# Kernel optimization log

Hardware: AMD Instinct MI355X
Metric: run time of the kernel (lower is better)

## Reference

```python
import jax, jax.numpy as jnp
import numpy as np
import math

D = 256; H = 8; L = 4; P = 4; DH = D // H; DF = 1024
B = 16; Q = 512
T_SHAPES = [8192, 4096, 2048, 1024]
LSI = [0, 8192, 12288, 14336]
S = sum(T_SHAPES)
EPS = 1e-5


def ln(x, w, b):
    m = jnp.mean(x, -1, keepdims=True)
    v = jnp.mean((x - m) ** 2, -1, keepdims=True)
    return (x - m) / jnp.sqrt(v + EPS) * w + b


def mha(q, k, v, valid, in_w, in_b, out_w, out_b):
    b_, n, _ = q.shape
    wq, wk, wv = jnp.split(in_w, 3, axis=0)
    bq, bk, bv = jnp.split(in_b, 3)
    qh = (q @ wq.T + bq).reshape(b_, n, H, DH).transpose(0, 2, 1, 3)
    kh = (k @ wk.T + bk).reshape(b_, n, H, DH).transpose(0, 2, 1, 3)
    vh = (v @ wv.T + bv).reshape(b_, n, H, DH).transpose(0, 2, 1, 3)
    s = jnp.einsum('bhqd,bhkd->bhqk', qh, kh) / math.sqrt(DH)
    s = jnp.where(valid[:, None, None, :], s, -1e30)
    a = jax.nn.softmax(s, -1)
    o = jnp.einsum('bhqk,bhkd->bhqd', a, vh).transpose(0, 2, 1, 3).reshape(b_, n, D)
    return o @ out_w.T + out_b


def msda(query, ref, src, pad_mask, ow, ob, aw, ab, vw, vb, pw, pb):
    # 1D multiscale deformable attention (PDVC-style), grid_sample semantics
    # with align_corners=False and zero padding.
    b_, s_, _ = src.shape
    q_ = query.shape[1]
    val = jnp.where(pad_mask[..., None], 0.0, src @ vw.T + vb).reshape(b_, s_, H, DH)
    off = (query @ ow.T + ob).reshape(b_, q_, H, L, P)
    attn = jax.nn.softmax((query @ aw.T + ab).reshape(b_, q_, H, L * P), -1)
    attn = attn.reshape(b_, q_, H, L, P)
    shapes = jnp.asarray(T_SHAPES, query.dtype)
    # (b,q,H,L,P) normalized sampling locations in [0,1]
    loc = ref[:, :, None, :, None, 0] + off / shapes[None, None, None, :, None]
    out = jnp.zeros((b_, q_, H, DH), query.dtype)
    for l in range(L):
        T = T_SHAPES[l]
        v = val[:, LSI[l]:LSI[l] + T].transpose(0, 2, 1, 3)  # (b,H,T,DH)
        x = loc[:, :, :, l, :] * T - 0.5  # pixel coords (b,q,H,P)
        x0 = jnp.floor(x)
        w = x - x0
        i0 = x0.astype(jnp.int32)
        i1 = i0 + 1
        m0 = ((i0 >= 0) & (i0 < T)).astype(query.dtype)
        m1 = ((i1 >= 0) & (i1 < T)).astype(query.dtype)

        def gather(idx):
            idxr = jnp.clip(idx, 0, T - 1).transpose(0, 2, 1, 3).reshape(b_, H, q_ * P)
            g = jnp.take_along_axis(v, idxr[..., None], axis=2)  # (b,H,q*P,DH)
            return g.reshape(b_, H, q_, P, DH).transpose(0, 2, 1, 3, 4)

        samp = gather(i0) * (m0 * (1.0 - w))[..., None] + gather(i1) * (m1 * w)[..., None]
        out = out + jnp.einsum('bqhp,bqhpd->bqhd', attn[:, :, :, l, :], samp)
    return out.reshape(b_, q_, D) @ pw.T + pb, loc[..., None], attn


def layer_fwd(tgt, query_pos, ref_v, ref_a, query_mask, vsrc, vpad, asrc, apad, p):
    qk = tgt + query_pos
    t2 = mha(qk, qk, tgt, query_mask, p['sa_in_w'], p['sa_in_b'], p['sa_out_w'], p['sa_out_b'])
    t = ln(tgt + t2, p['n2_w'], p['n2_b'])
    qv = t + query_pos
    ca_args = (p['ca_off_w'], p['ca_off_b'], p['ca_attn_w'], p['ca_attn_b'],
               p['ca_val_w'], p['ca_val_b'], p['ca_out_w'], p['ca_out_b'])
    cv, vloc, vattn = msda(qv, ref_v, vsrc, vpad, *ca_args)
    tv = ln(t + cv, p['n1_w'], p['n1_b'])
    ca, aloc, aattn = msda(qv, ref_a, asrc, apad, *ca_args)
    ta = ln(t + ca, p['n1_w'], p['n1_b'])
    cat = ln(jnp.concatenate([tv, ta], -1), p['n4_w'], p['n4_b'])
    x = jax.nn.relu(cat @ p['lin3_w'].T + p['lin3_b'])
    ff = jax.nn.relu(x @ p['lin1_w'].T + p['lin1_b']) @ p['lin2_w'].T + p['lin2_b']
    out = ln(x + ff, p['n3_w'], p['n3_b'])
    return out, tv, ta, vloc, vattn, aloc, aattn


def setup_inputs() -> dict:
    key = jax.random.key(0)
    ks = jax.random.split(key, 24)
    g = lambda k, shp: (jax.random.normal(k, shp, jnp.float32) * 0.02)
    inp = {
        'tgt': jax.random.normal(ks[0], (B, Q, D), jnp.float32),
        'query_pos': jax.random.normal(ks[1], (B, Q, D), jnp.float32),
        'reference_points_input_video': jax.random.uniform(ks[2], (B, Q, L, 1), jnp.float32),
        'reference_points_input_audio': jax.random.uniform(ks[3], (B, Q, L, 1), jnp.float32),
        'query_mask': jnp.ones((B, Q), bool),
        'video_src': jax.random.normal(ks[4], (B, S, D), jnp.float32),
        'video_temporal_shapes': jnp.asarray(T_SHAPES, jnp.int64),
        'video_level_start_index': jnp.asarray(LSI, jnp.int64),
        'video_src_padding_mask': jnp.zeros((B, S), bool),
        'audio_src': jax.random.normal(ks[5], (B, S, D), jnp.float32),
        'audio_temporal_shapes': jnp.asarray(T_SHAPES, jnp.int64),
        'audio_level_start_index': jnp.asarray(LSI, jnp.int64),
        'audio_src_padding_mask': jnp.zeros((B, S), bool),
        'sa_in_w': g(ks[6], (3 * D, D)), 'sa_in_b': jnp.zeros((3 * D,), jnp.float32),
        'sa_out_w': g(ks[7], (D, D)), 'sa_out_b': jnp.zeros((D,), jnp.float32),
        'ca_off_w': g(ks[8], (H * L * P, D)), 'ca_off_b': jax.random.uniform(ks[9], (H * L * P,), jnp.float32, -4.0, 4.0),
        'ca_attn_w': g(ks[10], (H * L * P, D)), 'ca_attn_b': jnp.zeros((H * L * P,), jnp.float32),
        'ca_val_w': g(ks[11], (D, D)), 'ca_val_b': jnp.zeros((D,), jnp.float32),
        'ca_out_w': g(ks[12], (D, D)), 'ca_out_b': jnp.zeros((D,), jnp.float32),
        'n1_w': jnp.ones((D,), jnp.float32), 'n1_b': jnp.zeros((D,), jnp.float32),
        'n2_w': jnp.ones((D,), jnp.float32), 'n2_b': jnp.zeros((D,), jnp.float32),
        'n3_w': jnp.ones((D,), jnp.float32), 'n3_b': jnp.zeros((D,), jnp.float32),
        'n4_w': jnp.ones((2 * D,), jnp.float32), 'n4_b': jnp.zeros((2 * D,), jnp.float32),
        'lin1_w': g(ks[13], (DF, D)), 'lin1_b': jnp.zeros((DF,), jnp.float32),
        'lin2_w': g(ks[14], (D, DF)), 'lin2_b': jnp.zeros((D,), jnp.float32),
        'lin3_w': g(ks[15], (D, 2 * D)), 'lin3_b': jnp.zeros((D,), jnp.float32),
    }
    return inp


def reference(tgt, query_pos, reference_points_input_video, reference_points_input_audio,
              query_mask, video_src, video_temporal_shapes, video_level_start_index,
              video_src_padding_mask, audio_src, audio_temporal_shapes,
              audio_level_start_index, audio_src_padding_mask,
              sa_in_w, sa_in_b, sa_out_w, sa_out_b,
              ca_off_w, ca_off_b, ca_attn_w, ca_attn_b, ca_val_w, ca_val_b, ca_out_w, ca_out_b,
              n1_w, n1_b, n2_w, n2_b, n3_w, n3_b, n4_w, n4_b,
              lin1_w, lin1_b, lin2_w, lin2_b, lin3_w, lin3_b):
    p = dict(sa_in_w=sa_in_w, sa_in_b=sa_in_b, sa_out_w=sa_out_w, sa_out_b=sa_out_b,
             ca_off_w=ca_off_w, ca_off_b=ca_off_b, ca_attn_w=ca_attn_w, ca_attn_b=ca_attn_b,
             ca_val_w=ca_val_w, ca_val_b=ca_val_b, ca_out_w=ca_out_w, ca_out_b=ca_out_b,
             n1_w=n1_w, n1_b=n1_b, n2_w=n2_w, n2_b=n2_b, n3_w=n3_w, n3_b=n3_b,
             n4_w=n4_w, n4_b=n4_b, lin1_w=lin1_w, lin1_b=lin1_b,
             lin2_w=lin2_w, lin2_b=lin2_b, lin3_w=lin3_w, lin3_b=lin3_b)
    return layer_fwd(tgt, query_pos, reference_points_input_video,
                     reference_points_input_audio, query_mask,
                     video_src, video_src_padding_mask,
                     audio_src, audio_src_padding_mask, p)
```

## Files before the change

### kernel.cpp

```cpp
#include <hip/hip_runtime.h>
#include <hip/hip_bf16.h>
#include <cstddef>

#define Dm   256
#define Hh   8
#define Bb   16
#define Qq   512
#define Ss   15360
#define TOK  (Bb*Qq)
#define VROWS (Bb*Ss)
#define EPSf 1e-5f
#define SCALEf 0.17677669529663687f

typedef __attribute__((ext_vector_type(8))) short bf16x8;
typedef __attribute__((ext_vector_type(4))) float f32x4;

__device__ __forceinline__ unsigned short rne_bf16(float f) {
    unsigned int u = __builtin_bit_cast(unsigned int, f);
    u += 0x7fffu + ((u >> 16) & 1u);
    return (unsigned short)(u >> 16);
}
__device__ __forceinline__ float bf2f(unsigned short u) {
    return __builtin_bit_cast(float, (unsigned int)u << 16);
}

struct WcArgs { const float* src[9]; };

__global__ __launch_bounds__(256) void wconv_kernel(
    WcArgs a, unsigned short* __restrict__ dst,
    const float* __restrict__ offb, const float* __restrict__ attnb,
    float* __restrict__ bias_oa)
{
    if (blockIdx.x == 1088) {
        int t = threadIdx.x;
        bias_oa[t] = (t < 128) ? offb[t] : attnb[t - 128];
        return;
    }
    int g = blockIdx.x * 256 + threadIdx.x;
    const int pre[10] = {0, 49152, 65536, 73728, 81920, 98304, 114688, 147456, 212992, 278528};
    int seg = 0;
    #pragma unroll
    for (int s2 = 1; s2 < 9; ++s2) seg += (g >= pre[s2]);
    float4 f = reinterpret_cast<const float4*>(a.src[seg])[g - pre[seg]];
    ushort4 o;
    o.x = rne_bf16(f.x); o.y = rne_bf16(f.y);
    o.z = rne_bf16(f.z); o.w = rne_bf16(f.w);
    reinterpret_cast<ushort4*>(dst)[g] = o;
}

template<int BM, int BN, bool RELU, bool ABF, bool OBF, bool ADD, bool SPLITA>
__global__ __launch_bounds__(512) void gemm_mfma_kernel(
    const void* __restrict__ Ap, const void* __restrict__ Ap2,
    const float* __restrict__ A2,
    const unsigned short* __restrict__ W,
    const float* __restrict__ bias, void* __restrict__ Cp,
    int M, int N, int K, int Msplit)
{
    constexpr int MI = BM / 32;
    constexpr int NI = BN / 64;
    __shared__ unsigned short As[BM * 32];
    __shared__ unsigned short Bs[BN * 32];
    const int tid = threadIdx.x, wid = tid >> 6, lane = tid & 63;
    const int wr = wid >> 2, wc = wid & 3;
    const int bm = blockIdx.x * BM, bn = blockIdx.y * BN;
    const int l15 = lane & 15, l4 = lane >> 4;
    const void* Ause = Ap;
    int bmA = bm;
    if (SPLITA && bm >= Msplit) { Ause = Ap2; bmA = bm - Msplit; }
    f32x4 acc[MI][NI] = {};

    for (int k0 = 0; k0 < K; k0 += 32) {
        __syncthreads();
        if (ABF) {
            const unsigned short* A = (const unsigned short*)Ause;
            constexpr int CH = BM * 4;
            #pragma unroll
            for (int i = 0; i < (CH + 511) / 512; ++i) {
                int idx = i * 512 + tid;
                if ((CH % 512) && idx >= CH) break;
                int row = idx >> 2, c = idx & 3;
                int4 a4 = *reinterpret_cast<const int4*>(&A[(size_t)(bmA + row) * K + k0 + c * 8]);
                *reinterpret_cast<int4*>(reinterpret_cast<char*>(As)
                    + row * 64 + ((c ^ (row & 3)) << 4)) = a4;
            }
        } else {
            const float* A = (const float*)Ause;
            constexpr int CH = BM * 8;
            #pragma unroll
            for (int i = 0; i < CH / 512; ++i) {
                int idx = i * 512 + tid;
                int row = idx >> 3, c4 = idx & 7;
                size_t g = (size_t)(bmA + row) * K + k0 + c4 * 4;
                float4 a4 = *reinterpret_cast<const float4*>(&A[g]);
                if (ADD) {
                    float4 b4 = *reinterpret_cast<const float4*>(
                        &A2[(size_t)(bm + row) * K + k0 + c4 * 4]);
                    a4.x += b4.x; a4.y += b4.y; a4.z += b4.z; a4.w += b4.w;
                }
                ushort4 u;
                u.x = rne_bf16(a4.x); u.y = rne_bf16(a4.y);
                u.z = rne_bf16(a4.z); u.w = rne_bf16(a4.w);
                *reinterpret_cast<ushort4*>(reinterpret_cast<char*>(As)
                    + row * 64 + (((c4 >> 1) ^ (row & 3)) << 4) + (c4 & 1) * 8) = u;
            }
        }
        {
            constexpr int CH = BN * 4;
            #pragma unroll
            for (int i = 0; i < CH / 512; ++i) {
                int idx = i * 512 + tid;
                int row = idx >> 2, c = idx & 3;
                int4 w4 = *reinterpret_cast<const int4*>(&W[(size_t)(bn + row) * K + k0 + c * 8]);
                *reinterpret_cast<int4*>(reinterpret_cast<char*>(Bs)
                    + row * 64 + ((c ^ (row & 3)) << 4)) = w4;
            }
        }
        __syncthreads();
        bf16x8 af[MI], bfr[NI];
        #pragma unroll
        for (int i = 0; i < MI; ++i) {
            int r = wr * (BM / 2) + i * 16 + l15;
            af[i] = *reinterpret_cast<const bf16x8*>(
                reinterpret_cast<const char*>(As) + r * 64 + ((l4 ^ (r & 3)) << 4));
        }
        #pragma unroll
        for (int j = 0; j < NI; ++j) {
            int r = wc * (BN / 4) + j * 16 + l15;
            bfr[j] = *reinterpret_cast<const bf16x8*>(
                reinterpret_cast<const char*>(Bs) + r * 64 + ((l4 ^ (r & 3)) << 4));
        }
        #pragma unroll
        for (int i = 0; i < MI; ++i)
            #pragma unroll
            for (int j = 0; j < NI; ++j)
                acc[i][j] = __builtin_amdgcn_mfma_f32_16x16x32_bf16(
                    af[i], bfr[j], acc[i][j], 0, 0, 0);
    }
    #pragma unroll
    for (int j = 0; j < NI; ++j) {
        int col = bn + wc * (BN / 4) + j * 16 + l15;
        float bv = bias[col];
        #pragma unroll
        for (int i = 0; i < MI; ++i) {
            int row0 = bm + wr * (BM / 2) + i * 16 + l4 * 4;
            #pragma unroll
            for (int v = 0; v < 4; ++v) {
                float val = acc[i][j][v] + bv;
                if (RELU) val = fmaxf(val, 0.f);
                if (OBF)
                    ((unsigned short*)Cp)[(size_t)(row0 + v) * N + col] = rne_bf16(val);
                else
                    ((float*)Cp)[(size_t)(row0 + v) * N + col] = val;
            }
        }
    }
}

template<int BM, bool DUAL>
__global__ __launch_bounds__(512) void gemm_ln_kernel(
    const unsigned short* __restrict__ A,
    const unsigned short* __restrict__ W,
    const float* __restrict__ bias,
    const float* __restrict__ res,
    const float* __restrict__ lnw, const float* __restrict__ lnb,
    float* __restrict__ out0, float* __restrict__ out1,
    int M, int K)
{
    constexpr int MI = BM / 32;
    constexpr int NI = 4;
    __shared__ unsigned short As[BM * 32];
    __shared__ unsigned short Bs[256 * 32];
    __shared__ float redS[BM][4];
    __shared__ float redQ[BM][4];
    const int tid = threadIdx.x, wid = tid >> 6, lane = tid & 63;
    const int wr = wid >> 2, wc = wid & 3;
    const int bm = blockIdx.x * BM;
    const int l15 = lane & 15, l4 = lane >> 4;
    f32x4 acc[MI][NI] = {};

    for (int k0 = 0; k0 < K; k0 += 32) {
        __syncthreads();
        {
            constexpr int CH = BM * 4;
            #pragma unroll
            for (int i = 0; i < (CH + 511) / 512; ++i) {
                int idx = i * 512 + tid;
                if ((CH % 512) && idx >= CH) break;
                int row = idx >> 2, c = idx & 3;
                int4 a4 = *reinterpret_cast<const int4*>(&A[(size_t)(bm + row) * K + k0 + c * 8]);
                *reinterpret_cast<int4*>(reinterpret_cast<char*>(As)
                    + row * 64 + ((c ^ (row & 3)) << 4)) = a4;
            }
        }
        {
            #pragma unroll
            for (int i = 0; i < 2; ++i) {
                int idx = i * 512 + tid;
                int row = idx >> 2, c = idx & 3;
                int4 w4 = *reinterpret_cast<const int4*>(&W[(size_t)row * K + k0 + c * 8]);
                *reinterpret_cast<int4*>(reinterpret_cast<char*>(Bs)
                    + row * 64 + ((c ^ (row & 3)) << 4)) = w4;
            }
        }
        __syncthreads();
        bf16x8 af[MI], bfr[NI];
        #pragma unroll
        for (int i = 0; i < MI; ++i) {
            int r = wr * (BM / 2) + i * 16 + l15;
            af[i] = *reinterpret_cast<const bf16x8*>(
                reinterpret_cast<const char*>(As) + r * 64 + ((l4 ^ (r & 3)) << 4));
        }
        #pragma unroll
        for (int j = 0; j < NI; ++j) {
            int r = wc * 64 + j * 16 + l15;
            bfr[j] = *reinterpret_cast<const bf16x8*>(
                reinterpret_cast<const char*>(Bs) + r * 64 + ((l4 ^ (r & 3)) << 4));
        }
        #pragma unroll
        for (int i = 0; i < MI; ++i)
            #pragma unroll
            for (int j = 0; j < NI; ++j)
                acc[i][j] = __builtin_amdgcn_mfma_f32_16x16x32_bf16(
                    af[i], bfr[j], acc[i][j], 0, 0, 0);
    }

    const bool hi = DUAL && (bm >= (M >> 1));
    const int bmL = hi ? bm - (M >> 1) : bm;
    float* outp = (DUAL && hi) ? out1 : out0;

    #pragma unroll
    for (int i = 0; i < MI; ++i) {
        #pragma unroll
        for (int v = 0; v < 4; ++v) {
            int rloc = wr * (BM / 2) + i * 16 + l4 * 4 + v;
            size_t rrow = (size_t)(bmL + rloc) * 256;
            float s = 0.f, q = 0.f;
            #pragma unroll
            for (int j = 0; j < NI; ++j) {
                int col = wc * 64 + j * 16 + l15;
                float x = acc[i][j][v] + bias[col] + res[rrow + col];
                acc[i][j][v] = x;
                s += x; q += x * x;
            }
            #pragma unroll
            for (int msk = 1; msk < 16; msk <<= 1) {
                s += __shfl_xor(s, msk, 64);
                q += __shfl_xor(q, msk, 64);
            }
            if (l15 == 0) { redS[rloc][wc] = s; redQ[rloc][wc] = q; }
        }
    }
    __syncthreads();
    #pragma unroll
    for (int i = 0; i < MI; ++i) {
        #pragma unroll
        for (int v = 0; v < 4; ++v) {
            int rloc = wr * (BM / 2) + i * 16 + l4 * 4 + v;
            float S = redS[rloc][0] + redS[rloc][1] + redS[rloc][2] + redS[rloc][3];
            float Qs = redQ[rloc][0] + redQ[rloc][1] + redQ[rloc][2] + redQ[rloc][3];
            float mean = S * (1.f / 256.f);
            float var = Qs * (1.f / 256.f) - mean * mean;
            float rinv = rsqrtf(var + EPSf);
            size_t rrow = (size_t)(bmL + rloc) * 256;
            #pragma unroll
            for (int j = 0; j < NI; ++j) {
                int col = wc * 64 + j * 16 + l15;
                outp[rrow + col] = (acc[i][j][v] - mean) * rinv * lnw[col] + lnb[col];
            }
        }
    }
}

__global__ __launch_bounds__(512) void gemm_prep_kernel(
    const float* __restrict__ A, const float* __restrict__ A2,
    const unsigned short* __restrict__ W, const float* __restrict__ bias,
    const float* __restrict__ refv, const float* __restrict__ refa,
    float* __restrict__ vloc, float* __restrict__ vattn,
    float* __restrict__ aloc, float* __restrict__ aattn)
{
    constexpr int BM = 64, MI = 2, NI = 4;
    const int K = 256;
    __shared__ unsigned short As[BM * 32];
    __shared__ unsigned short Bs[256 * 32];
    const int tid = threadIdx.x, wid = tid >> 6, lane = tid & 63;
    const int wr = wid >> 2, wc = wid & 3;
    const int bm = blockIdx.x * BM;
    const int l15 = lane & 15, l4 = lane >> 4;
    f32x4 acc[MI][NI] = {};

    for (int k0 = 0; k0 < K; k0 += 32) {
        __syncthreads();
        {
            int idx = tid;
            int row = idx >> 3, c4 = idx & 7;
            size_t g = (size_t)(bm + row) * K + k0 + c4 * 4;
            float4 a4 = *reinterpret_cast<const float4*>(&A[g]);
            float4 b4 = *reinterpret_cast<const float4*>(&A2[g]);
            a4.x += b4.x; a4.y += b4.y; a4.z += b4.z; a4.w += b4.w;
            ushort4 u;
            u.x = rne_bf16(a4.x); u.y = rne_bf16(a4.y);
            u.z = rne_bf16(a4.z); u.w = rne_bf16(a4.w);
            *reinterpret_cast<ushort4*>(reinterpret_cast<char*>(As)
                + row * 64 + (((c4 >> 1) ^ (row & 3)) << 4) + (c4 & 1) * 8) = u;
        }
        {
            #pragma unroll
            for (int i = 0; i < 2; ++i) {
                int idx = i * 512 + tid;
                int row = idx >> 2, c = idx & 3;
                int4 w4 = *reinterpret_cast<const int4*>(&W[(size_t)row * K + k0 + c * 8]);
                *reinterpret_cast<int4*>(reinterpret_cast<char*>(Bs)
                    + row * 64 + ((c ^ (row & 3)) << 4)) = w4;
            }
        }
        __syncthreads();
        bf16x8 af[MI], bfr[NI];
        #pragma unroll
        for (int i = 0; i < MI; ++i) {
            int r = wr * 32 + i * 16 + l15;
            af[i] = *reinterpret_cast<const bf16x8*>(
                reinterpret_cast<const char*>(As) + r * 64 + ((l4 ^ (r & 3)) << 4));
        }
        #pragma unroll
        for (int j = 0; j < NI; ++j) {
            int r = wc * 64 + j * 16 + l15;
            bfr[j] = *reinterpret_cast<const bf16x8*>(
                reinterpret_cast<const char*>(Bs) + r * 64 + ((l4 ^ (r & 3)) << 4));
        }
        #pragma unroll
        for (int i = 0; i < MI; ++i)
            #pragma unroll
            for (int j = 0; j < NI; ++j)
                acc[i][j] = __builtin_amdgcn_mfma_f32_16x16x32_bf16(
                    af[i], bfr[j], acc[i][j], 0, 0, 0);
    }

    const float invT[4] = {1.f/8192.f, 1.f/4096.f, 1.f/2048.f, 1.f/1024.f};
    const int l = (l15 >> 2) & 3;
    if (wc < 2) {
        #pragma unroll
        for (int i = 0; i < MI; ++i) {
            #pragma unroll
            for (int v = 0; v < 4; ++v) {
                int tok = bm + wr * 32 + i * 16 + l4 * 4 + v;
                float rv = refv[(size_t)tok * 4 + l];
                float ra = refa[(size_t)tok * 4 + l];
                #pragma unroll
                for (int j = 0; j < NI; ++j) {
                    int col = wc * 64 + j * 16 + l15;
                    float off = (acc[i][j][v] + bias[col]) * invT[l];
                    vloc[(size_t)tok * 128 + col] = rv + off;
                    aloc[(size_t)tok * 128 + col] = ra + off;
                }
            }
        }
    } else {
        #pragma unroll
        for (int i = 0; i < MI; ++i) {
            #pragma unroll
            for (int v = 0; v < 4; ++v) {
                int tok = bm + wr * 32 + i * 16 + l4 * 4 + v;
                #pragma unroll
                for (int j = 0; j < NI; ++j) {
                    int col = wc * 64 + j * 16 + l15;
                    float lg = acc[i][j][v] + bias[col];
                    float m = lg;
                    #pragma unroll
                    for (int msk = 1; msk < 16; msk <<= 1)
                        m = fmaxf(m, __shfl_xor(m, msk, 64));
                    float e = __expf(lg - m);
                    float s = e;
                    #pragma unroll
                    for (int msk = 1; msk < 16; msk <<= 1)
                        s += __shfl_xor(s, msk, 64);
                    float at = e / s;
                    int c = col - 128;
                    vattn[(size_t)tok * 128 + c] = at;
                    aattn[(size_t)tok * 128 + c] = at;
                }
            }
        }
    }
}

__global__ __launch_bounds__(256) void sa_flash_kernel(
    const unsigned short* __restrict__ qkh, const unsigned short* __restrict__ vh,
    unsigned short* __restrict__ o)
{
    const int qt = blockIdx.x & 3;
    const int h  = (blockIdx.x >> 2) & 7;
    const int b  = blockIdx.x >> 5;
    const int tid = threadIdx.x;
    const int wid = tid >> 6;
    const int lane = tid & 63;
    const int l15 = lane & 15, l4 = lane >> 4;

    __shared__ unsigned short Ks[64 * 32];
    __shared__ unsigned short Vt[32 * 64];
    __shared__ unsigned short Ps[4][32 * 64];

    const int qbase = qt * 128 + wid * 32;
    bf16x8 qf[2];
    #pragma unroll
    for (int i = 0; i < 2; ++i) {
        int row = b * 512 + qbase + i * 16 + l15;
        qf[i] = *reinterpret_cast<const bf16x8*>(&qkh[(size_t)row * 512 + h * 32 + l4 * 8]);
    }

    f32x4 oacc[2][2] = {};
    float m_r[8], l_r[8];
    #pragma unroll
    for (int i = 0; i < 8; ++i) { m_r[i] = -1e30f; l_r[i] = 0.f; }

    for (int kt = 0; kt < 8; ++kt) {
        __syncthreads();
        {
            int row = tid >> 2, c = tid & 3;
            int4 k4 = *reinterpret_cast<const int4*>(
                &qkh[(size_t)(b * 512 + kt * 64 + row) * 512 + 256 + h * 32 + c * 8]);
            *reinterpret_cast<int4*>(reinterpret_cast<char*>(Ks)
                + row * 64 + ((c ^ (row & 3)) << 4)) = k4;
        }
        {
            int k = tid >> 2, dh0 = (tid & 3) * 8;
            const unsigned short* vp = &vh[(size_t)(b * 512 + kt * 64 + k) * 256 + h * 32 + dh0];
            ushort4 v0 = *reinterpret_cast<const ushort4*>(vp);
            ushort4 v1 = *reinterpret_cast<const ushort4*>(vp + 4);
            unsigned short vv[8] = {v0.x, v0.y, v0.z, v0.w, v1.x, v1.y, v1.z, v1.w};
            int kc = k >> 3, kb = (k & 7) * 2;
            #pragma unroll
            for (int j = 0; j < 8; ++j) {
                int dh = dh0 + j;
                *reinterpret_cast<unsigned short*>(reinterpret_cast<char*>(Vt)
                    + dh * 128 + ((kc ^ (dh & 7)) << 4) + kb) = vv[j];
            }
        }
        __syncthreads();

        bf16x8 kf[4];
        #pragma unroll
        for (int j = 0; j < 4; ++j) {
            int r = j * 16 + l15;
            kf[j] = *reinterpret_cast<const bf16x8*>(
                reinterpret_cast<const char*>(Ks) + r * 64 + ((l4 ^ (r & 3)) << 4));
        }
        f32x4 s[2][4];
        #pragma unroll
        for (int i = 0; i < 2; ++i)
            #pragma unroll
            for (int j = 0; j < 4; ++j) {
                f32x4 z = {0.f, 0.f, 0.f, 0.f};
                s[i][j] = __builtin_amdgcn_mfma_f32_16x16x32_bf16(qf[i], kf[j], z, 0, 0, 0);
            }

        #pragma unroll
        for (int i = 0; i < 2; ++i) {
            #pragma unroll
            for (int reg = 0; reg < 4; ++reg) {
                float v0 = s[i][0][reg] * SCALEf;
                float v1 = s[i][1][reg] * SCALEf;
                float v2 = s[i][2][reg] * SCALEf;
                float v3 = s[i][3][reg] * SCALEf;
                float mx = fmaxf(fmaxf(v0, v1), fmaxf(v2, v3));
                #pragma unroll
                for (int d = 1; d < 16; d <<= 1) mx = fmaxf(mx, __shfl_xor(mx, d, 64));
                int idx = i * 4 + reg;
                float mnew = fmaxf(m_r[idx], mx);
                float alpha = __expf(m_r[idx] - mnew);
                float p0 = __expf(v0 - mnew), p1 = __expf(v1 - mnew);
                float p2 = __expf(v2 - mnew), p3 = __expf(v3 - mnew);
                float rs = (p0 + p1) + (p2 + p3);
                #pragma unroll
                for (int d = 1; d < 16; d <<= 1) rs += __shfl_xor(rs, d, 64);
                l_r[idx] = l_r[idx] * alpha + rs;
                m_r[idx] = mnew;
                oacc[i][0][reg] *= alpha;
                oacc[i][1][reg] *= alpha;
                int row = i * 16 + l4 * 4 + reg;
                char* pbase = reinterpret_cast<char*>(Ps[wid]) + row * 128 + (l15 & 7) * 2;
                int ch = l15 >> 3;
                unsigned short pb[4] = {rne_bf16(p0), rne_bf16(p1), rne_bf16(p2), rne_bf16(p3)};
                #pragma unroll
                for (int j = 0; j < 4; ++j)
                    *reinterpret_cast<unsigned short*>(
                        pbase + (((j * 2 + ch) ^ (row & 7)) << 4)) = pb[j];
            }
        }
        asm volatile("s_waitcnt lgkmcnt(0)" ::: "memory");
        __builtin_amdgcn_sched_barrier(0);

        #pragma unroll
        for (int ks = 0; ks < 2; ++ks) {
            bf16x8 vf[2], pf[2];
            #pragma unroll
            for (int jd = 0; jd < 2; ++jd) {
                int r = jd * 16 + l15;
                vf[jd] = *reinterpret_cast<const bf16x8*>(
                    reinterpret_cast<const char*>(Vt) + r * 128 + (((ks * 4 + l4) ^ (r & 7)) << 4));
            }
            #pragma unroll
            for (int i = 0; i < 2; ++i) {
                int r = i * 16 + l15;
                pf[i] = *reinterpret_cast<const bf16x8*>(
                    reinterpret_cast<const char*>(Ps[wid]) + r * 128 + (((ks * 4 + l4) ^ (r & 7)) << 4));
            }
            #pragma unroll
            for (int i = 0; i < 2; ++i)
                #pragma unroll
                for (int jd = 0; jd < 2; ++jd)
                    oacc[i][jd] = __builtin_amdgcn_mfma_f32_16x16x32_bf16(
                        pf[i], vf[jd], oacc[i][jd], 0, 0, 0);
        }
    }

    #pragma unroll
    for (int i = 0; i < 2; ++i)
        #pragma unroll
        for (int reg = 0; reg < 4; ++reg) {
            int idx = i * 4 + reg;
            float inv = 1.f / l_r[idx];
            int qrow = b * 512 + qbase + i * 16 + l4 * 4 + reg;
            #pragma unroll
            for (int jd = 0; jd < 2; ++jd)
                o[(size_t)qrow * 256 + h * 32 + jd * 16 + l15] =
                    rne_bf16(oacc[i][jd][reg] * inv);
        }
}

__global__ __launch_bounds__(256) void cat_ln_kernel(
    const float* __restrict__ tv, const float* __restrict__ ta,
    const float* __restrict__ w, const float* __restrict__ beta,
    unsigned short* __restrict__ out)
{
    const int tok = blockIdx.x;
    const int t = threadIdx.x;
    const float x0 = tv[(size_t)tok * 256 + t];
    const float x1 = ta[(size_t)tok * 256 + t];
    __shared__ float red[8];
    float s = x0 + x1;
    #pragma unroll
    for (int k = 32; k > 0; k >>= 1) s += __shfl_xor(s, k, 64);
    if ((t & 63) == 0) red[t >> 6] = s;
    __syncthreads();
    const float mean = (red[0] + red[1] + red[2] + red[3]) * (1.f / 512.f);
    const float d0 = x0 - mean, d1 = x1 - mean;
    float v = d0 * d0 + d1 * d1;
    #pragma unroll
    for (int k = 32; k > 0; k >>= 1) v += __shfl_xor(v, k, 64);
    if ((t & 63) == 0) red[4 + (t >> 6)] = v;
    __syncthreads();
    const float var = (red[4] + red[5] + red[6] + red[7]) * (1.f / 512.f);
    const float r = 1.f / sqrtf(var + EPSf);
    out[(size_t)tok * 512 + t]       = rne_bf16(d0 * r * w[t] + beta[t]);
    out[(size_t)tok * 512 + 256 + t] = rne_bf16(d1 * r * w[256 + t] + beta[256 + t]);
}

__global__ __launch_bounds__(256) void msda_sample_kernel(
    const unsigned short* __restrict__ val,
    const float* __restrict__ vloc, const float* __restrict__ vattn,
    const float* __restrict__ aloc, const float* __restrict__ aattn,
    unsigned short* __restrict__ out)
{
    const int t = threadIdx.x;
    const int tq = t >> 6;
    const int h  = (t >> 3) & 7;
    const int d4 = t & 7;
    const int tok2 = blockIdx.x * 4 + tq;
    const int mod = tok2 >> 13;
    const int tok = tok2 & 8191;
    const int b = tok >> 9;
    const float* loc  = mod ? aloc  : vloc;
    const float* attn = mod ? aattn : vattn;
    const unsigned short* vbase = val + (size_t)mod * VROWS * 256
                                + (size_t)b * Ss * 256 + h * 32 + d4 * 4;
    const int Tt[4]   = {8192, 4096, 2048, 1024};
    const int LSIc[4] = {0, 8192, 12288, 14336};
    float4 acc = {0.f, 0.f, 0.f, 0.f};
    #pragma unroll
    for (int l = 0; l < 4; ++l) {
        const unsigned short* vl = vbase + (size_t)LSIc[l] * 256;
        const int T = Tt[l];
        #pragma unroll
        for (int p = 0; p < 4; ++p) {
            const int e = (h * 4 + l) * 4 + p;
            const float lc = loc[(size_t)tok * 128 + e];
            const float at = attn[(size_t)tok * 128 + e];
            const float x = lc * (float)T - 0.5f;
            const float x0 = floorf(x);
            const float w = x - x0;
            const int i0 = (int)x0;
            const int i1 = i0 + 1;
            const float w0 = (i0 >= 0 && i0 < T) ? at * (1.f - w) : 0.f;
            const float w1 = (i1 >= 0 && i1 < T) ? at * w : 0.f;
            const int i0c = min(max(i0, 0), T - 1);
            const int i1c = min(max(i1, 0), T - 1);
            ushort4 g0 = *reinterpret_cast<const ushort4*>(&vl[(size_t)i0c * 256]);
            ushort4 g1 = *reinterpret_cast<const ushort4*>(&vl[(size_t)i1c * 256]);
            acc.x += w0 * bf2f(g0.x) + w1 * bf2f(g1.x);
            acc.y += w0 * bf2f(g0.y) + w1 * bf2f(g1.y);
            acc.z += w0 * bf2f(g0.z) + w1 * bf2f(g1.z);
            acc.w += w0 * bf2f(g0.w) + w1 * bf2f(g1.w);
        }
    }
    ushort4 ov;
    ov.x = rne_bf16(acc.x); ov.y = rne_bf16(acc.y);
    ov.z = rne_bf16(acc.z); ov.w = rne_bf16(acc.w);
    *reinterpret_cast<ushort4*>(&out[(size_t)tok2 * 256 + h * 32 + d4 * 4]) = ov;
}

extern "C" void kernel_launch(void* const* d_in, const int* in_sizes, int n_in,
                              void* d_out, int out_size, void* d_ws, size_t ws_size,
                              hipStream_t stream)
{
    (void)in_sizes; (void)n_in; (void)out_size; (void)ws_size;
    const float* tgt       = (const float*)d_in[0];
    const float* query_pos = (const float*)d_in[1];
    const float* ref_v     = (const float*)d_in[2];
    const float* ref_a     = (const float*)d_in[3];
    const float* video_src = (const float*)d_in[5];
    const float* audio_src = (const float*)d_in[9];
    const float* sa_in_w   = (const float*)d_in[13];
    const float* sa_in_b   = (const float*)d_in[14];
    const float* sa_out_w  = (const float*)d_in[15];
    const float* sa_out_b  = (const float*)d_in[16];
    const float* ca_off_w  = (const float*)d_in[17];
    const float* ca_off_b  = (const float*)d_in[18];
    const float* ca_attn_w = (const float*)d_in[19];
    const float* ca_attn_b = (const float*)d_in[20];
    const float* ca_val_w  = (const float*)d_in[21];
    const float* ca_val_b  = (const float*)d_in[22];
    const float* ca_out_w  = (const float*)d_in[23];
    const float* ca_out_b  = (const float*)d_in[24];
    const float* n1_w = (const float*)d_in[25];
    const float* n1_b = (const float*)d_in[26];
    const float* n2_w = (const float*)d_in[27];
    const float* n2_b = (const float*)d_in[28];
    const float* n3_w = (const float*)d_in[29];
    const float* n3_b = (const float*)d_in[30];
    const float* n4_w = (const float*)d_in[31];
    const float* n4_b = (const float*)d_in[32];
    const float* lin1_w = (const float*)d_in[33];
    const float* lin1_b = (const float*)d_in[34];
    const float* lin2_w = (const float*)d_in[35];
    const float* lin2_b = (const float*)d_in[36];
    const float* lin3_w = (const float*)d_in[37];
    const float* lin3_b = (const float*)d_in[38];

    float* out_main  = (float*)d_out;
    float* out_tv    = out_main + (size_t)TOK * 256;
    float* out_ta    = out_tv   + (size_t)TOK * 256;
    float* out_vloc  = out_ta   + (size_t)TOK * 256;
    float* out_vattn = out_vloc + (size_t)TOK * 128;
    float* out_aloc  = out_vattn+ (size_t)TOK * 128;
    float* out_aattn = out_aloc + (size_t)TOK * 128;

    char* base = (char*)d_ws;
    const size_t MB = 1024 * 1024;
    unsigned short* f_qkh = (unsigned short*)(base + 0);
    unsigned short* f_vh  = (unsigned short*)(base + 8*MB);
    unsigned short* f_o   = (unsigned short*)(base + 12*MB);
    unsigned short* f_samp= (unsigned short*)(base + 0);
    unsigned short* f_cat = (unsigned short*)(base + 8*MB);
    unsigned short* f_ffh = (unsigned short*)(base + 16*MB);
    float* f_t = (float*)(base + 32*MB);
    float* f_x = (float*)(base + 40*MB);
    unsigned short* f_val = (unsigned short*)(base + 48*MB);
    unsigned short* wb = (unsigned short*)(base + 300*MB);
    unsigned short* w_sa_in  = wb;
    unsigned short* w_sa_out = w_sa_in  + 768 * 256;
    unsigned short* w_oa     = w_sa_out + 256 * 256;
    unsigned short* w_val    = w_oa     + 256 * 256;
    unsigned short* w_caout  = w_val    + 256 * 256;
    unsigned short* w_lin3   = w_caout  + 256 * 256;
    unsigned short* w_lin1   = w_lin3   + 256 * 512;
    unsigned short* w_lin2   = w_lin1   + 1024 * 256;
    float* bias_oa = (float*)(w_lin2 + 256 * 1024);

    WcArgs wa;
    wa.src[0] = sa_in_w;  wa.src[1] = sa_out_w; wa.src[2] = ca_off_w;
    wa.src[3] = ca_attn_w;wa.src[4] = ca_val_w; wa.src[5] = ca_out_w;
    wa.src[6] = lin3_w;   wa.src[7] = lin1_w;   wa.src[8] = lin2_w;
    hipLaunchKernelGGL(wconv_kernel, dim3(1089), dim3(256), 0, stream,
                       wa, wb, ca_off_b, ca_attn_b, bias_oa);

    hipLaunchKernelGGL((gemm_mfma_kernel<64,128,false,false,true,true,false>),
                       dim3(128, 4), dim3(512), 0, stream,
                       tgt, nullptr, query_pos, w_sa_in, sa_in_b, f_qkh,
                       TOK, 512, 256, 0);
    hipLaunchKernelGGL((gemm_mfma_kernel<64,128,false,false,true,false,false>),
                       dim3(128, 2), dim3(512), 0, stream,
                       tgt, nullptr, nullptr, w_sa_in + (size_t)512 * 256,
                       sa_in_b + 512, f_vh, TOK, 256, 256, 0);
    hipLaunchKernelGGL(sa_flash_kernel, dim3(Bb * 32), dim3(256), 0, stream,
                       f_qkh, f_vh, f_o);
    hipLaunchKernelGGL((gemm_ln_kernel<32,false>), dim3(256), dim3(512), 0, stream,
                       f_o, w_sa_out, sa_out_b, tgt, n2_w, n2_b,
                       f_t, nullptr, TOK, 256);
    hipLaunchKernelGGL(gemm_prep_kernel, dim3(128), dim3(512), 0, stream,
                       f_t, query_pos, w_oa, bias_oa, ref_v, ref_a,
                       out_vloc, out_vattn, out_aloc, out_aattn);
    hipLaunchKernelGGL((gemm_mfma_kernel<128,256,false,false,true,false,true>),
                       dim3(2 * VROWS / 128, 1), dim3(512), 0, stream,
                       video_src, audio_src, nullptr, w_val, ca_val_b, f_val,
                       2 * VROWS, 256, 256, VROWS);
    hipLaunchKernelGGL(msda_sample_kernel, dim3(2 * TOK / 4), dim3(256), 0, stream,
                       f_val, out_vloc, out_vattn, out_aloc, out_aattn, f_samp);
    hipLaunchKernelGGL((gemm_ln_kernel<64,true>), dim3(256), dim3(512), 0, stream,
                       f_samp, w_caout, ca_out_b, f_t, n1_w, n1_b,
                       out_tv, out_ta, 2 * TOK, 256);
    hipLaunchKernelGGL(cat_ln_kernel, dim3(TOK), dim3(256), 0, stream,
                       out_tv, out_ta, n4_w, n4_b, f_cat);
    hipLaunchKernelGGL((gemm_mfma_kernel<64,128,true,true,false,false,false>),
                       dim3(128, 2), dim3(512), 0, stream,
                       f_cat, nullptr, nullptr, w_lin3, lin3_b, f_x,
                       TOK, 256, 512, 0);
    hipLaunchKernelGGL((gemm_mfma_kernel<128,256,true,false,true,false,false>),
                       dim3(64, 4), dim3(512), 0, stream,
                       f_x, nullptr, nullptr, w_lin1, lin1_b, f_ffh,
                       TOK, 1024, 256, 0);
    hipLaunchKernelGGL((gemm_ln_kernel<32,false>), dim3(256), dim3(512), 0, stream,
                       f_ffh, w_lin2, lin2_b, f_x, n3_w, n3_b,
                       out_main, nullptr, TOK, 1024);
}
```

Before: 437.0 us.

## Add streaming value-projection kernel with whole weight resident in LDS

```diff
diff --git a/kernel.cpp b/kernel.cpp
--- a/kernel.cpp
+++ b/kernel.cpp
@@ -46,6 +46,69 @@
     o.x = rne_bf16(f.x); o.y = rne_bf16(f.y);
     o.z = rne_bf16(f.z); o.w = rne_bf16(f.w);
     reinterpret_cast<ushort4*>(dst)[g] = o;
+}
+
+__global__ __launch_bounds__(1024, 4) void val_stream_kernel(
+    const float* __restrict__ Av, const float* __restrict__ Aa,
+    const unsigned short* __restrict__ W, const float* __restrict__ bias,
+    unsigned short* __restrict__ C)
+{
+    __shared__ unsigned short Ws[8 * 256 * 32];
+    const int tid = threadIdx.x;
+    #pragma unroll
+    for (int i = 0; i < 8; ++i) {
+        int g = i * 1024 + tid;
+        int r = g >> 5, q = g & 31;
+        int c = q >> 2, ck = q & 3;
+        int slot = ck ^ (r & 3) ^ ((r >> 2) & 3);
+        int4 w4 = reinterpret_cast<const int4*>(W)[g];
+        *reinterpret_cast<int4*>(reinterpret_cast<char*>(Ws)
+            + c * 16384 + r * 64 + (slot << 4)) = w4;
+    }
+    __syncthreads();
+
+    const int wid = tid >> 6, lane = tid & 63;
+    const int l15 = lane & 15, l4 = lane >> 4;
+    size_t grow = (size_t)blockIdx.x * 256 + wid * 16;
+    const float* A = Av;
+    size_t arow = grow;
+    if (grow >= (size_t)VROWS) { A = Aa; arow = grow - VROWS; }
+    const float* aptr = A + (arow + l15) * 256 + l4 * 8;
+
+    f32x4 acc[16] = {};
+    float4 a0 = *reinterpret_cast<const float4*>(aptr);
+    float4 a1 = *reinterpret_cast<const float4*>(aptr + 4);
+    #pragma unroll
+    for (int kc = 0; kc < 8; ++kc) {
+        float4 n0, n1;
+        if (kc < 7) {
+            n0 = *reinterpret_cast<const float4*>(aptr + (kc + 1) * 32);
+            n1 = *reinterpret_cast<const float4*>(aptr + (kc + 1) * 32 + 4);
+        }
+        bf16x8 af;
+        af[0] = (short)rne_bf16(a0.x); af[1] = (short)rne_bf16(a0.y);
+        af[2] = (short)rne_bf16(a0.z); af[3] = (short)rne_bf16(a0.w);
+        af[4] = (short)rne_bf16(a1.x); af[5] = (short)rne_bf16(a1.y);
+        af[6] = (short)rne_bf16(a1.z); af[7] = (short)rne_bf16(a1.w);
+        const char* wbase = reinterpret_cast<const char*>(Ws) + kc * 16384;
+        #pragma unroll
+        for (int n = 0; n < 16; ++n) {
+            int r = n * 16 + l15;
+            int slot = l4 ^ (r & 3) ^ ((r >> 2) & 3);
+            bf16x8 bf = *reinterpret_cast<const bf16x8*>(wbase + r * 64 + (slot << 4));
+            acc[n] = __builtin_amdgcn_mfma_f32_16x16x32_bf16(af, bf, acc[n], 0, 0, 0);
+        }
+        if (kc < 7) { a0 = n0; a1 = n1; }
+    }
+    #pragma unroll
+    for (int n = 0; n < 16; ++n) {
+        int col = n * 16 + l15;
+        float bv = bias[col];
+        size_t r0 = grow + l4 * 4;
+        #pragma unroll
+        for (int v = 0; v < 4; ++v)
+            C[(r0 + v) * 256 + col] = rne_bf16(acc[n][v] + bv);
+    }
 }
 
 template<int BM, int BN, bool RELU, bool ABF, bool OBF, bool ADD, bool SPLITA>
@@ -699,10 +762,8 @@
     hipLaunchKernelGGL(gemm_prep_kernel, dim3(128), dim3(512), 0, stream,
                        f_t, query_pos, w_oa, bias_oa, ref_v, ref_a,
                        out_vloc, out_vattn, out_aloc, out_aattn);
-    hipLaunchKernelGGL((gemm_mfma_kernel<128,256,false,false,true,false,true>),
-                       dim3(2 * VROWS / 128, 1), dim3(512), 0, stream,
-                       video_src, audio_src, nullptr, w_val, ca_val_b, f_val,
-                       2 * VROWS, 256, 256, VROWS);
+    hipLaunchKernelGGL(val_stream_kernel, dim3(2 * VROWS / 256), dim3(1024), 0, stream,
+                       video_src, audio_src, w_val, ca_val_b, f_val);
     hipLaunchKernelGGL(msda_sample_kernel, dim3(2 * TOK / 4), dim3(256), 0, stream,
                        f_val, out_vloc, out_vattn, out_aloc, out_aattn, f_samp);
     hipLaunchKernelGGL((gemm_ln_kernel<64,true>), dim3(256), dim3(512), 0, stream,
```

After: 399.2 us. 8.7% less time.

## Replace value-projection GEMM with persistent streaming kernel holding weights in registers

Applied to the files above, without the earlier changes.

```diff
diff --git a/kernel.cpp b/kernel.cpp
--- a/kernel.cpp
+++ b/kernel.cpp
@@ -46,6 +46,98 @@
     o.x = rne_bf16(f.x); o.y = rne_bf16(f.y);
     o.z = rne_bf16(f.z); o.w = rne_bf16(f.w);
     reinterpret_cast<ushort4*>(dst)[g] = o;
+}
+
+__global__ __launch_bounds__(512, 2) void val_stream_kernel(
+    const float* __restrict__ Av, const float* __restrict__ Aa,
+    const unsigned short* __restrict__ W, const float* __restrict__ bias,
+    unsigned short* __restrict__ C)
+{
+    const int tid = threadIdx.x, wid = tid >> 6, lane = tid & 63;
+    const int l15 = lane & 15, l4 = lane >> 4;
+    const int rg = wid >> 2;
+    const int cg = wid & 3;
+
+    bf16x8 wf[4][8];
+    #pragma unroll
+    for (int j = 0; j < 4; ++j)
+        #pragma unroll
+        for (int kc = 0; kc < 8; ++kc)
+            wf[j][kc] = *reinterpret_cast<const bf16x8*>(
+                &W[(size_t)(cg * 64 + j * 16 + l15) * 256 + kc * 32 + l4 * 8]);
+    float4 bb[4];
+    #pragma unroll
+    for (int j = 0; j < 4; ++j)
+        bb[j] = *reinterpret_cast<const float4*>(&bias[cg * 64 + j * 16 + l4 * 4]);
+
+    int t = blockIdx.x;
+    const float* ap;
+    {
+        size_t grow = (size_t)t * 32;
+        const float* A = (grow < (size_t)VROWS) ? Av : Aa;
+        size_t ar = (grow < (size_t)VROWS) ? grow : grow - VROWS;
+        ap = A + (ar + rg * 16 + l15) * 256 + l4 * 8;
+    }
+
+    float4 b0[4], b1[4];
+    #define LOADQ(buf, base, ph) {                                          \
+        buf[0] = *reinterpret_cast<const float4*>((base) + (ph) * 64);      \
+        buf[1] = *reinterpret_cast<const float4*>((base) + (ph) * 64 + 4);  \
+        buf[2] = *reinterpret_cast<const float4*>((base) + (ph) * 64 + 32); \
+        buf[3] = *reinterpret_cast<const float4*>((base) + (ph) * 64 + 36); }
+    #define COMPQ(buf, kc0) {                                               \
+        bf16x8 a0, a1;                                                      \
+        a0[0] = (short)rne_bf16(buf[0].x); a0[1] = (short)rne_bf16(buf[0].y); \
+        a0[2] = (short)rne_bf16(buf[0].z); a0[3] = (short)rne_bf16(buf[0].w); \
+        a0[4] = (short)rne_bf16(buf[1].x); a0[5] = (short)rne_bf16(buf[1].y); \
+        a0[6] = (short)rne_bf16(buf[1].z); a0[7] = (short)rne_bf16(buf[1].w); \
+        acc[0] = __builtin_amdgcn_mfma_f32_16x16x32_bf16(wf[0][kc0], a0, acc[0], 0, 0, 0); \
+        acc[1] = __builtin_amdgcn_mfma_f32_16x16x32_bf16(wf[1][kc0], a0, acc[1], 0, 0, 0); \
+        acc[2] = __builtin_amdgcn_mfma_f32_16x16x32_bf16(wf[2][kc0], a0, acc[2], 0, 0, 0); \
+        acc[3] = __builtin_amdgcn_mfma_f32_16x16x32_bf16(wf[3][kc0], a0, acc[3], 0, 0, 0); \
+        a1[0] = (short)rne_bf16(buf[2].x); a1[1] = (short)rne_bf16(buf[2].y); \
+        a1[2] = (short)rne_bf16(buf[2].z); a1[3] = (short)rne_bf16(buf[2].w); \
+        a1[4] = (short)rne_bf16(buf[3].x); a1[5] = (short)rne_bf16(buf[3].y); \
+        a1[6] = (short)rne_bf16(buf[3].z); a1[7] = (short)rne_bf16(buf[3].w); \
+        acc[0] = __builtin_amdgcn_mfma_f32_16x16x32_bf16(wf[0][kc0 + 1], a1, acc[0], 0, 0, 0); \
+        acc[1] = __builtin_amdgcn_mfma_f32_16x16x32_bf16(wf[1][kc0 + 1], a1, acc[1], 0, 0, 0); \
+        acc[2] = __builtin_amdgcn_mfma_f32_16x16x32_bf16(wf[2][kc0 + 1], a1, acc[2], 0, 0, 0); \
+        acc[3] = __builtin_amdgcn_mfma_f32_16x16x32_bf16(wf[3][kc0 + 1], a1, acc[3], 0, 0, 0); }
+
+    LOADQ(b0, ap, 0);
+    #pragma unroll 1
+    for (int i = 0; i < 8; ++i) {
+        const int tn = t + 1920;
+        const float* apn = ap;
+        if (i < 7) {
+            size_t grow = (size_t)tn * 32;
+            const float* A = (grow < (size_t)VROWS) ? Av : Aa;
+            size_t ar = (grow < (size_t)VROWS) ? grow : grow - VROWS;
+            apn = A + (ar + rg * 16 + l15) * 256 + l4 * 8;
+        }
+        f32x4 acc[4];
+        #pragma unroll
+        for (int j = 0; j < 4; ++j) {
+            acc[j][0] = bb[j].x; acc[j][1] = bb[j].y;
+            acc[j][2] = bb[j].z; acc[j][3] = bb[j].w;
+        }
+        LOADQ(b1, ap, 1);  COMPQ(b0, 0);
+        LOADQ(b0, ap, 2);  COMPQ(b1, 2);
+        LOADQ(b1, ap, 3);  COMPQ(b0, 4);
+        LOADQ(b0, apn, 0); COMPQ(b1, 6);
+        size_t rrow = (size_t)t * 32 + rg * 16 + l15;
+        #pragma unroll
+        for (int j = 0; j < 4; ++j) {
+            ushort4 o;
+            o.x = rne_bf16(acc[j][0]); o.y = rne_bf16(acc[j][1]);
+            o.z = rne_bf16(acc[j][2]); o.w = rne_bf16(acc[j][3]);
+            *reinterpret_cast<ushort4*>(
+                &C[rrow * 256 + cg * 64 + j * 16 + l4 * 4]) = o;
+        }
+        t = tn; ap = apn;
+    }
+    #undef LOADQ
+    #undef COMPQ
 }
 
 template<int BM, int BN, bool RELU, bool ABF, bool OBF, bool ADD, bool SPLITA>
@@ -699,10 +791,8 @@
     hipLaunchKernelGGL(gemm_prep_kernel, dim3(128), dim3(512), 0, stream,
                        f_t, query_pos, w_oa, bias_oa, ref_v, ref_a,
                        out_vloc, out_vattn, out_aloc, out_aattn);
-    hipLaunchKernelGGL((gemm_mfma_kernel<128,256,false,false,true,false,true>),
-                       dim3(2 * VROWS / 128, 1), dim3(512), 0, stream,
-                       video_src, audio_src, nullptr, w_val, ca_val_b, f_val,
-                       2 * VROWS, 256, 256, VROWS);
+    hipLaunchKernelGGL(val_stream_kernel, dim3(1920), dim3(512), 0, stream,
+                       video_src, audio_src, w_val, ca_val_b, f_val);
     hipLaunchKernelGGL(msda_sample_kernel, dim3(2 * TOK / 4), dim3(256), 0, stream,
                        f_val, out_vloc, out_vattn, out_aloc, out_aattn, f_samp);
     hipLaunchKernelGGL((gemm_ln_kernel<64,true>), dim3(256), dim3(512), 0, stream,
```

New measurement: 584.7 us. 33.8% more time.

## Aggregate raw MSDA source rows before projecting values per head

Applied to the files above, without the earlier changes.

```diff
diff --git a/kernel.cpp b/kernel.cpp
--- a/kernel.cpp
+++ b/kernel.cpp
@@ -46,6 +46,111 @@
     o.x = rne_bf16(f.x); o.y = rne_bf16(f.y);
     o.z = rne_bf16(f.z); o.w = rne_bf16(f.w);
     reinterpret_cast<ushort4*>(dst)[g] = o;
+}
+
+__global__ __launch_bounds__(256) void msda_agg_kernel(
+    const float* __restrict__ vsrc, const float* __restrict__ asrc,
+    const float* __restrict__ vloc, const float* __restrict__ vattn,
+    const float* __restrict__ aloc, const float* __restrict__ aattn,
+    unsigned short* __restrict__ agg, float* __restrict__ sumw)
+{
+    __shared__ float sl[128], sa[128];
+    const int blk = blockIdx.x;
+    const int mod = blk >> 13, tok = blk & 8191, b = tok >> 9;
+    const float* loc  = mod ? aloc  : vloc;
+    const float* attn = mod ? aattn : vattn;
+    const float* src  = (mod ? asrc : vsrc) + (size_t)b * Ss * 256;
+    const int t = threadIdx.x;
+    if (t < 128) sl[t] = loc[(size_t)tok * 128 + t];
+    else         sa[t - 128] = attn[(size_t)tok * 128 + (t - 128)];
+    __syncthreads();
+    const int g = t >> 6, lane = t & 63;
+    const int Tt[4]   = {8192, 4096, 2048, 1024};
+    const int LSIc[4] = {0, 8192, 12288, 14336};
+    #pragma unroll
+    for (int hh = 0; hh < 2; ++hh) {
+        const int h = g * 2 + hh;
+        float4 acc = {0.f, 0.f, 0.f, 0.f};
+        float sw = 0.f;
+        #pragma unroll
+        for (int l = 0; l < 4; ++l) {
+            const float* vl = src + (size_t)LSIc[l] * 256 + lane * 4;
+            const int T = Tt[l];
+            #pragma unroll
+            for (int p = 0; p < 4; ++p) {
+                const int e = h * 16 + l * 4 + p;
+                const float lc = sl[e], at = sa[e];
+                const float x = lc * (float)T - 0.5f;
+                const float x0 = floorf(x);
+                const float w = x - x0;
+                const int i0 = (int)x0;
+                const int i1 = i0 + 1;
+                const float w0 = (i0 >= 0 && i0 < T) ? at * (1.f - w) : 0.f;
+                const float w1 = (i1 >= 0 && i1 < T) ? at * w : 0.f;
+                sw += w0 + w1;
+                const int i0c = min(max(i0, 0), T - 1);
+                const int i1c = min(max(i1, 0), T - 1);
+                float4 g0 = *reinterpret_cast<const float4*>(vl + (size_t)i0c * 256);
+                float4 g1 = *reinterpret_cast<const float4*>(vl + (size_t)i1c * 256);
+                acc.x += w0 * g0.x + w1 * g1.x;
+                acc.y += w0 * g0.y + w1 * g1.y;
+                acc.z += w0 * g0.z + w1 * g1.z;
+                acc.w += w0 * g0.w + w1 * g1.w;
+            }
+        }
+        const size_t row = (size_t)h * 16384 + blk;
+        ushort4 o;
+        o.x = rne_bf16(acc.x); o.y = rne_bf16(acc.y);
+        o.z = rne_bf16(acc.z); o.w = rne_bf16(acc.w);
+        *reinterpret_cast<ushort4*>(&agg[row * 256 + lane * 4]) = o;
+        if (lane == 0) sumw[row] = sw;
+    }
+}
+
+__global__ __launch_bounds__(256) void agg_proj_kernel(
+    const unsigned short* __restrict__ agg, const float* __restrict__ sumw,
+    const unsigned short* __restrict__ W, const float* __restrict__ bias,
+    unsigned short* __restrict__ samp)
+{
+    const int tid = threadIdx.x, wv = tid >> 6, lane = tid & 63;
+    const int l15 = lane & 15, l4 = lane >> 4;
+    const int h = blockIdx.y;
+    const int bm = blockIdx.x * 64;
+
+    bf16x8 wf[2][8];
+    #pragma unroll
+    for (int n = 0; n < 2; ++n)
+        #pragma unroll
+        for (int kc = 0; kc < 8; ++kc)
+            wf[n][kc] = *reinterpret_cast<const bf16x8*>(
+                &W[(size_t)(h * 32 + n * 16 + l15) * 256 + kc * 32 + l4 * 8]);
+    float4 bv[2];
+    #pragma unroll
+    for (int n = 0; n < 2; ++n)
+        bv[n] = *reinterpret_cast<const float4*>(&bias[h * 32 + n * 16 + l4 * 4]);
+
+    const size_t slab = (size_t)h * 16384;
+    const int r0 = bm + wv * 16;
+    const unsigned short* ap = &agg[(slab + r0 + l15) * 256 + l4 * 8];
+    const float srow = sumw[slab + r0 + l15];
+
+    f32x4 acc[2] = {};
+    #pragma unroll
+    for (int kc = 0; kc < 8; ++kc) {
+        bf16x8 af = *reinterpret_cast<const bf16x8*>(ap + kc * 32);
+        acc[0] = __builtin_amdgcn_mfma_f32_16x16x32_bf16(wf[0][kc], af, acc[0], 0, 0, 0);
+        acc[1] = __builtin_amdgcn_mfma_f32_16x16x32_bf16(wf[1][kc], af, acc[1], 0, 0, 0);
+    }
+    #pragma unroll
+    for (int n = 0; n < 2; ++n) {
+        ushort4 o;
+        o.x = rne_bf16(acc[n][0] + bv[n].x * srow);
+        o.y = rne_bf16(acc[n][1] + bv[n].y * srow);
+        o.z = rne_bf16(acc[n][2] + bv[n].z * srow);
+        o.w = rne_bf16(acc[n][3] + bv[n].w * srow);
+        *reinterpret_cast<ushort4*>(
+            &samp[(size_t)(r0 + l15) * 256 + h * 32 + n * 16 + l4 * 4]) = o;
+    }
 }
 
 template<int BM, int BN, bool RELU, bool ABF, bool OBF, bool ADD, bool SPLITA>
@@ -553,59 +658,6 @@
     const float r = 1.f / sqrtf(var + EPSf);
     out[(size_t)tok * 512 + t]       = rne_bf16(d0 * r * w[t] + beta[t]);
     out[(size_t)tok * 512 + 256 + t] = rne_bf16(d1 * r * w[256 + t] + beta[256 + t]);
-}
-
-__global__ __launch_bounds__(256) void msda_sample_kernel(
-    const unsigned short* __restrict__ val,
-    const float* __restrict__ vloc, const float* __restrict__ vattn,
-    const float* __restrict__ aloc, const float* __restrict__ aattn,
-    unsigned short* __restrict__ out)
-{
-    const int t = threadIdx.x;
-    const int tq = t >> 6;
-    const int h  = (t >> 3) & 7;
-    const int d4 = t & 7;
-    const int tok2 = blockIdx.x * 4 + tq;
-    const int mod = tok2 >> 13;
-    const int tok = tok2 & 8191;
-    const int b = tok >> 9;
-    const float* loc  = mod ? aloc  : vloc;
-    const float* attn = mod ? aattn : vattn;
-    const unsigned short* vbase = val + (size_t)mod * VROWS * 256
-                                + (size_t)b * Ss * 256 + h * 32 + d4 * 4;
-    const int Tt[4]   = {8192, 4096, 2048, 1024};
-    const int LSIc[4] = {0, 8192, 12288, 14336};
-    float4 acc = {0.f, 0.f, 0.f, 0.f};
-    #pragma unroll
-    for (int l = 0; l < 4; ++l) {
-        const unsigned short* vl = vbase + (size_t)LSIc[l] * 256;
-        const int T = Tt[l];
-        #pragma unroll
-        for (int p = 0; p < 4; ++p) {
-            const int e = (h * 4 + l) * 4 + p;
-            const float lc = loc[(size_t)tok * 128 + e];
-            const float at = attn[(size_t)tok * 128 + e];
-            const float x = lc * (float)T - 0.5f;
-            const float x0 = floorf(x);
-            const float w = x - x0;
-            const int i0 = (int)x0;
-            const int i1 = i0 + 1;
-            const float w0 = (i0 >= 0 && i0 < T) ? at * (1.f - w) : 0.f;
-            const float w1 = (i1 >= 0 && i1 < T) ? at * w : 0.f;
-            const int i0c = min(max(i0, 0), T - 1);
-            const int i1c = min(max(i1, 0), T - 1);
-            ushort4 g0 = *reinterpret_cast<const ushort4*>(&vl[(size_t)i0c * 256]);
-            ushort4 g1 = *reinterpret_cast<const ushort4*>(&vl[(size_t)i1c * 256]);
-            acc.x += w0 * bf2f(g0.x) + w1 * bf2f(g1.x);
-            acc.y += w0 * bf2f(g0.y) + w1 * bf2f(g1.y);
-            acc.z += w0 * bf2f(g0.z) + w1 * bf2f(g1.z);
-            acc.w += w0 * bf2f(g0.w) + w1 * bf2f(g1.w);
-        }
-    }
-    ushort4 ov;
-    ov.x = rne_bf16(acc.x); ov.y = rne_bf16(acc.y);
-    ov.z = rne_bf16(acc.z); ov.w = rne_bf16(acc.w);
-    *reinterpret_cast<ushort4*>(&out[(size_t)tok2 * 256 + h * 32 + d4 * 4]) = ov;
 }
 
 extern "C" void kernel_launch(void* const* d_in, const int* in_sizes, int n_in,
@@ -664,8 +716,9 @@
     unsigned short* f_ffh = (unsigned short*)(base + 16*MB);
     float* f_t = (float*)(base + 32*MB);
     float* f_x = (float*)(base + 40*MB);
-    unsigned short* f_val = (unsigned short*)(base + 48*MB);
-    unsigned short* wb = (unsigned short*)(base + 300*MB);
+    unsigned short* f_agg = (unsigned short*)(base + 48*MB);
+    float* f_sumw = (float*)(base + 112*MB);
+    unsigned short* wb = (unsigned short*)(base + 120*MB);
     unsigned short* w_sa_in  = wb;
     unsigned short* w_sa_out = w_sa_in  + 768 * 256;
     unsigned short* w_oa     = w_sa_out + 256 * 256;
@@ -699,12 +752,12 @@
     hipLaunchKernelGGL(gemm_prep_kernel, dim3(128), dim3(512), 0, stream,
                        f_t, query_pos, w_oa, bias_oa, ref_v, ref_a,
                        out_vloc, out_vattn, out_aloc, out_aattn);
-    hipLaunchKernelGGL((gemm_mfma_kernel<128,256,false,false,true,false,true>),
-                       dim3(2 * VROWS / 128, 1), dim3(512), 0, stream,
-                       video_src, audio_src, nullptr, w_val, ca_val_b, f_val,
-                       2 * VROWS, 256, 256, VROWS);
-    hipLaunchKernelGGL(msda_sample_kernel, dim3(2 * TOK / 4), dim3(256), 0, stream,
-                       f_val, out_vloc, out_vattn, out_aloc, out_aattn, f_samp);
+    hipLaunchKernelGGL(msda_agg_kernel, dim3(2 * TOK), dim3(256), 0, stream,
+                       video_src, audio_src,
+                       out_vloc, out_vattn, out_aloc, out_aattn,
+                       f_agg, f_sumw);
+    hipLaunchKernelGGL(agg_proj_kernel, dim3(2 * TOK / 64, 8), dim3(256), 0, stream,
+                       f_agg, f_sumw, w_val, ca_val_b, f_samp);
     hipLaunchKernelGGL((gemm_ln_kernel<64,true>), dim3(256), dim3(512), 0, stream,
                        f_samp, w_caout, ca_out_b, f_t, n1_w, n1_b,
                        out_tv, out_ta, 2 * TOK, 256);
```

Result: slower. 462.1 us (+5.7%).
